# Kernel optimization log

Measured on AMD Instinct MI355X. Metric: run time of the kernel, lower is better.

The kernel has to match this reference:

```python
import jax, jax.numpy as jnp
import numpy as np

D_MODEL, D_K, D_V = 1024, 64, 64

def setup_inputs() -> dict:
    key = jax.random.key(0)
    ks = jax.random.split(key, 9)
    B, S = 8, 2048
    scale = 1.0 / np.sqrt(D_MODEL)
    return {
        "q_input": jax.random.normal(ks[0], (B, S, D_MODEL), jnp.float32),
        "k_input": jax.random.normal(ks[1], (B, S, D_MODEL), jnp.float32),
        "v_input": jax.random.normal(ks[2], (B, S, D_MODEL), jnp.float32),
        "Wq": jax.random.normal(ks[3], (D_K, D_MODEL), jnp.float32) * scale,
        "bq": jnp.zeros((D_K,), jnp.float32),
        "Wk": jax.random.normal(ks[4], (D_K, D_MODEL), jnp.float32) * scale,
        "bk": jnp.zeros((D_K,), jnp.float32),
        "Wv": jax.random.normal(ks[5], (D_V, D_MODEL), jnp.float32) * scale,
        "bv": jnp.zeros((D_V,), jnp.float32),
    }

def reference(q_input, k_input, v_input, Wq, bq, Wk, bk, Wv, bv):
    # Linear projections (torch Linear: x @ W^T + b)
    q = jnp.einsum('bsm,km->bsk', q_input, Wq) + bq  # [B,S,d_k]
    k = jnp.einsum('bsm,km->bsk', k_input, Wk) + bk  # [B,S,d_k]
    v = jnp.einsum('bsm,vm->bsv', v_input, Wv) + bv  # [B,S,d_v]
    scores = jnp.einsum('bqk,bsk->bqs', q, k) / jnp.sqrt(jnp.float32(D_K))
    # source applies causal mask unconditionally (is_mask is never None)
    S = q_input.shape[1]
    causal = jnp.tril(jnp.ones((S, S), bool))
    scores = jnp.where(causal[None], scores, jnp.float32(-1e9))
    attn = jax.nn.softmax(scores, axis=2)
    return jnp.einsum('bqs,bsv->bqv', attn, v)
```

## Files before the change

### kernel.cpp

```cpp
#include <hip/hip_runtime.h>
#include <hip/hip_bf16.h>

#define B_ 8
#define S_ 2048
#define DM 1024
#define DK 64

typedef __attribute__((ext_vector_type(8))) short bf16x8;
typedef __attribute__((ext_vector_type(4))) float f32x4;
typedef __attribute__((ext_vector_type(4))) short short4_t;
typedef unsigned int u32;

__device__ __forceinline__ short bf16s(float f) {
    union { float f; unsigned u; } v; v.f = f;
    unsigned r = v.u + 0x7fffu + ((v.u >> 16) & 1u);
    return (short)(r >> 16);
}

__global__ __launch_bounds__(256) void convw_kernel(
    const float* __restrict__ Wq, const float* __restrict__ Wk,
    const float* __restrict__ Wv, short* __restrict__ wbf)
{
    const int i = (blockIdx.x * 256 + threadIdx.x) * 8;
    const float* src = (i < 65536) ? Wq : (i < 131072) ? Wk : Wv;
    const int off = i & 65535;
    float4 f0 = *(const float4*)(src + off);
    float4 f1 = *(const float4*)(src + off + 4);
    bf16x8 o;
    o[0]=bf16s(f0.x); o[1]=bf16s(f0.y); o[2]=bf16s(f0.z); o[3]=bf16s(f0.w);
    o[4]=bf16s(f1.x); o[5]=bf16s(f1.y); o[6]=bf16s(f1.z); o[7]=bf16s(f1.w);
    *(bf16x8*)(wbf + i) = o;
}

__global__ __launch_bounds__(256) void proj_kernel(
    const float* __restrict__ xq, const float* __restrict__ xk, const float* __restrict__ xv,
    const short* __restrict__ wbf,
    const float* __restrict__ bq, const float* __restrict__ bk, const float* __restrict__ bv,
    short* __restrict__ q_ws, short* __restrict__ k_ws, short* __restrict__ vt_ws)
{
    __shared__ __align__(16) char smem[49152];

    const int which = blockIdx.y;
    const float* x    = (which == 0) ? xq : (which == 1) ? xk : xv;
    const float* bias = (which == 0) ? bq : (which == 1) ? bk : bv;
    const short* wsrc = wbf + which * (DK * DM);

    const int tid = threadIdx.x;
    const int w   = tid >> 6;
    const int i   = tid & 63;
    const int lr  = i & 15;
    const int g   = i >> 4;
    const int row0 = blockIdx.x * 64;

    const int rot = (blockIdx.x * 5 + which * 7) & 15;

    f32x4 acc[4];
    #pragma unroll
    for (int f = 0; f < 4; ++f) acc[f] = f32x4{0.f, 0.f, 0.f, 0.f};

    auto fetch = [&](f32x4 (&xb)[4], f32x4 (&wb)[2], int kc) {
        const float* xrow = x + (long)(row0 + w * 16) * DM + kc;
        #pragma unroll
        for (int j = 0; j < 4; ++j) {
            const int rl = j * 4 + g;
            xb[j] = __builtin_nontemporal_load(
                (const f32x4*)((const char*)(xrow + (long)rl * DM) + (i & 15) * 16));
        }
        const short* wrow = wsrc + (long)(w * 16) * DM + kc;
        #pragma unroll
        for (int j = 0; j < 2; ++j) {
            const int nl = j * 8 + (i >> 3);
            wb[j] = *(const f32x4*)((const char*)(wrow + (long)nl * DM) + (i & 7) * 16);
        }
    };
    auto writeLDS = [&](const f32x4 (&xb)[4], const f32x4 (&wb)[2], int buf) {
        char* xd = smem + buf * 16384 + (w * 16) * 256;
        #pragma unroll
        for (int j = 0; j < 4; ++j) {
            const int rl = j * 4 + g;
            *(f32x4*)(xd + rl * 256 + (((i & 15) * 16) ^ ((rl & 7) << 5))) = xb[j];
        }
        char* wd = smem + 32768 + buf * 8192 + (w * 16) * 128;
        #pragma unroll
        for (int j = 0; j < 2; ++j) {
            const int nl = j * 8 + (i >> 3);
            *(f32x4*)(wd + nl * 128 + (((i & 7) * 16) ^ ((nl & 7) << 4))) = wb[j];
        }
    };

    auto compute = [&](int buf) {
        const char* xr = smem + buf * 16384 + (w * 16 + lr) * 256;
        const char* wr = smem + 32768 + buf * 8192;
        const int sx = (lr & 7) << 5;
        const int sw = (lr & 7) << 4;
        #pragma unroll
        for (int ks = 0; ks < 2; ++ks) {
            const int bA = (ks * 128 + g * 32) ^ sx;
            f32x4 x0 = *(const f32x4*)(xr + bA);
            f32x4 x1 = *(const f32x4*)(xr + bA + 16);
            bf16x8 af;
            af[0]=bf16s(x0[0]); af[1]=bf16s(x0[1]); af[2]=bf16s(x0[2]); af[3]=bf16s(x0[3]);
            af[4]=bf16s(x1[0]); af[5]=bf16s(x1[1]); af[6]=bf16s(x1[2]); af[7]=bf16s(x1[3]);
            const int bB = (ks * 64 + g * 16) ^ sw;
            #pragma unroll
            for (int f = 0; f < 4; ++f) {
                bf16x8 wf = *(const bf16x8*)(wr + (f * 16 + lr) * 128 + bB);
                acc[f] = __builtin_amdgcn_mfma_f32_16x16x32_bf16(af, wf, acc[f], 0, 0, 0);
            }
        }
    };

    f32x4 xA[4], wA[2], xB[4], wB[2];
    fetch(xA, wA, rot * 64);
    writeLDS(xA, wA, 0);
    fetch(xB, wB, ((1 + rot) & 15) * 64);
    asm volatile("s_waitcnt lgkmcnt(0)" ::: "memory");
    asm volatile("s_barrier" ::: "memory");

    for (int t = 0; t < 16; t += 2) {
        compute(0);
        if (t + 2 < 16) fetch(xA, wA, ((t + 2 + rot) & 15) * 64);
        writeLDS(xB, wB, 1);
        asm volatile("s_waitcnt lgkmcnt(0)" ::: "memory");
        asm volatile("s_barrier" ::: "memory");
        compute(1);
        if (t + 3 < 16) fetch(xB, wB, ((t + 3 + rot) & 15) * 64);
        if (t + 2 < 16) {
            writeLDS(xA, wA, 0);
            asm volatile("s_waitcnt lgkmcnt(0)" ::: "memory");
        }
        asm volatile("s_barrier" ::: "memory");
    }

    if (which < 2) {
        short* stile = (short*)smem + w * 1024;
        #pragma unroll
        for (int f = 0; f < 4; ++f) {
            float bb = bias[f * 16 + lr];
            #pragma unroll
            for (int r = 0; r < 4; ++r)
                stile[(g * 4 + r) * 64 + f * 16 + lr] = bf16s(acc[f][r] + bb);
        }
        asm volatile("s_waitcnt lgkmcnt(0)" ::: "memory");
        __builtin_amdgcn_sched_barrier(0);
        short* outp = (which == 0) ? q_ws : k_ws;
        const long gbase = (long)(row0 + w * 16) * 64;
        *(bf16x8*)(outp + gbase +       i * 8) = *(const bf16x8*)(&stile[i * 8]);
        *(bf16x8*)(outp + gbase + 512 + i * 8) = *(const bf16x8*)(&stile[512 + i * 8]);
    } else {
        const int rw = row0 + w * 16;
        const int b = rw >> 11;
        const int s = (rw & 2047) + g * 4;
        #pragma unroll
        for (int f = 0; f < 4; ++f) {
            float bb = bias[f * 16 + lr];
            short4_t st;
            st[0]=bf16s(acc[f][0]+bb); st[1]=bf16s(acc[f][1]+bb);
            st[2]=bf16s(acc[f][2]+bb); st[3]=bf16s(acc[f][3]+bb);
            *(short4_t*)(vt_ws + (long)(b * 64 + f * 16 + lr) * S_ + s) = st;
        }
    }
}

__global__ __launch_bounds__(256) void attn_kernel(
    const short* __restrict__ q_ws, const short* __restrict__ k_ws,
    const short* __restrict__ vt_ws, float* __restrict__ out)
{
    __shared__ __align__(16) short plds[4][16 * 40];
    __shared__ __align__(16) float accds[4][64][16];
    __shared__ __align__(16) float2 mlds[4][16];

    const int n = blockIdx.x;
    const int c = n & 255, s = n >> 8;
    const int u = c & 127, v = c >> 7;
    const int b  = v * 4 + s;
    const int qt = (s & 1) ? (127 - u) : u;
    const int qbase = qt * 16;
    const int kend  = qbase + 16;
    const int niter = (kend + 31) >> 5;

    const int tid  = threadIdx.x;
    const int wv   = tid >> 6;
    const int lane = tid & 63;
    const int lr = lane & 15, g = lane >> 4, lk = g * 8;
    const int q_glob = qbase + lr;

    const short* qp = q_ws + ((long)b * S_ + qbase + lr) * DK;
    const bf16x8 qb0 = *(const bf16x8*)(qp + lk);
    const bf16x8 qb1 = *(const bf16x8*)(qp + 32 + lk);
    const short* kb = k_ws  + (long)b * S_ * DK;
    const short* vb = vt_ws + (long)b * DK * S_;

    float m = -INFINITY, l = 0.f;
    f32x4 acc[4];
    #pragma unroll
    for (int f = 0; f < 4; ++f) acc[f] = f32x4{0.f, 0.f, 0.f, 0.f};
    const float sc = 0.125f * 1.44269504088896340736f;

    short* pw = plds[wv];
    for (int t = wv; t < niter; t += 4) {
        const int kv = t * 32;
        const bool sub1 = (kv + 16) < kend;
        bf16x8 vf0 = *(const bf16x8*)(vb + (long)(lr)      * S_ + kv + lk);
        bf16x8 vf1 = *(const bf16x8*)(vb + (long)(16 + lr) * S_ + kv + lk);
        bf16x8 vf2 = *(const bf16x8*)(vb + (long)(32 + lr) * S_ + kv + lk);
        bf16x8 vf3 = *(const bf16x8*)(vb + (long)(48 + lr) * S_ + kv + lk);

        const short* kp0 = kb + (long)(kv + lr) * DK;
        bf16x8 k00 = *(const bf16x8*)(kp0 + lk);
        bf16x8 k01 = *(const bf16x8*)(kp0 + 32 + lk);
        f32x4 s0 = f32x4{0.f,0.f,0.f,0.f};
        s0 = __builtin_amdgcn_mfma_f32_16x16x32_bf16(k00, qb0, s0, 0, 0, 0);
        s0 = __builtin_amdgcn_mfma_f32_16x16x32_bf16(k01, qb1, s0, 0, 0, 0);
        f32x4 s1 = f32x4{0.f,0.f,0.f,0.f};
        if (sub1) {
            const short* kp1 = kp0 + 16 * DK;
            bf16x8 k10 = *(const bf16x8*)(kp1 + lk);
            bf16x8 k11 = *(const bf16x8*)(kp1 + 32 + lk);
            s1 = __builtin_amdgcn_mfma_f32_16x16x32_bf16(k10, qb0, s1, 0, 0, 0);
            s1 = __builtin_amdgcn_mfma_f32_16x16x32_bf16(k11, qb1, s1, 0, 0, 0);
        }

        float pv[8];
        #pragma unroll
        for (int r = 0; r < 4; ++r) {
            const int key0 = kv + g*4 + r;
            pv[r]     = (key0 <= q_glob) ? s0[r] * sc : -INFINITY;
            const int key1 = kv + 16 + g*4 + r;
            pv[4 + r] = (sub1 && key1 <= q_glob) ? s1[r] * sc : -INFINITY;
        }
        float tm = fmaxf(fmaxf(fmaxf(pv[0],pv[1]), fmaxf(pv[2],pv[3])),
                         fmaxf(fmaxf(pv[4],pv[5]), fmaxf(pv[6],pv[7])));
        tm = fmaxf(tm, __shfl_xor(tm, 16));
        tm = fmaxf(tm, __shfl_xor(tm, 32));
        const float mn  = fmaxf(m, tm);
        const float fac = exp2f(m - mn);
        float ps = 0.f;
        #pragma unroll
        for (int q = 0; q < 8; ++q) { pv[q] = exp2f(pv[q] - mn); ps += pv[q]; }
        ps += __shfl_xor(ps, 16);
        ps += __shfl_xor(ps, 32);
        l = l * fac + ps;
        m = mn;
        #pragma unroll
        for (int f = 0; f < 4; ++f)
            #pragma unroll
            for (int r = 0; r < 4; ++r) acc[f][r] *= fac;

        short4_t pw0, pw1;
        pw0[0]=bf16s(pv[0]); pw0[1]=bf16s(pv[1]); pw0[2]=bf16s(pv[2]); pw0[3]=bf16s(pv[3]);
        pw1[0]=bf16s(pv[4]); pw1[1]=bf16s(pv[5]); pw1[2]=bf16s(pv[6]); pw1[3]=bf16s(pv[7]);
        *(short4_t*)(pw + lr*40 + g*4)      = pw0;
        *(short4_t*)(pw + lr*40 + 16 + g*4) = pw1;
        asm volatile("s_waitcnt lgkmcnt(0)" ::: "memory");
        __builtin_amdgcn_sched_barrier(0);
        const bf16x8 pf = *(const bf16x8*)(pw + lr*40 + lk);

        acc[0] = __builtin_amdgcn_mfma_f32_16x16x32_bf16(vf0, pf, acc[0], 0, 0, 0);
        acc[1] = __builtin_amdgcn_mfma_f32_16x16x32_bf16(vf1, pf, acc[1], 0, 0, 0);
        acc[2] = __builtin_amdgcn_mfma_f32_16x16x32_bf16(vf2, pf, acc[2], 0, 0, 0);
        acc[3] = __builtin_amdgcn_mfma_f32_16x16x32_bf16(vf3, pf, acc[3], 0, 0, 0);
    }

    #pragma unroll
    for (int f = 0; f < 4; ++f)
        *(f32x4*)(&accds[wv][lane][f * 4]) = acc[f];
    if (g == 0) mlds[wv][lr] = float2{m, l};
    __syncthreads();

    const float2 ml0 = mlds[0][lr], ml1 = mlds[1][lr],
                 ml2 = mlds[2][lr], ml3 = mlds[3][lr];
    const float M = fmaxf(fmaxf(ml0.x, ml1.x), fmaxf(ml2.x, ml3.x));
    const float w0 = exp2f(ml0.x - M), w1 = exp2f(ml1.x - M),
                w2 = exp2f(ml2.x - M), w3 = exp2f(ml3.x - M);
    const float L = w0*ml0.y + w1*ml1.y + w2*ml2.y + w3*ml3.y;
    f32x4 o = w0 * (*(const f32x4*)(&accds[0][lane][wv * 4]))
            + w1 * (*(const f32x4*)(&accds[1][lane][wv * 4]))
            + w2 * (*(const f32x4*)(&accds[2][lane][wv * 4]))
            + w3 * (*(const f32x4*)(&accds[3][lane][wv * 4]));
    const float inv = 1.0f / L;
    o[0]*=inv; o[1]*=inv; o[2]*=inv; o[3]*=inv;
    *(f32x4*)(out + ((long)b * S_ + qbase + lr) * DK + wv * 16 + g * 4) = o;
}

extern "C" void kernel_launch(void* const* d_in, const int* in_sizes, int n_in,
                              void* d_out, int out_size, void* d_ws, size_t ws_size,
                              hipStream_t stream) {
    const float* q_in = (const float*)d_in[0];
    const float* k_in = (const float*)d_in[1];
    const float* v_in = (const float*)d_in[2];
    const float* Wq   = (const float*)d_in[3];
    const float* bq   = (const float*)d_in[4];
    const float* Wk   = (const float*)d_in[5];
    const float* bk   = (const float*)d_in[6];
    const float* Wv   = (const float*)d_in[7];
    const float* bv   = (const float*)d_in[8];

    short* q_ws  = (short*)d_ws;
    short* k_ws  = q_ws + (size_t)B_ * S_ * DK;
    short* vt_ws = k_ws + (size_t)B_ * S_ * DK;
    short* wbf   = vt_ws + (size_t)B_ * S_ * DK;
    float* out   = (float*)d_out;

    convw_kernel<<<dim3(96), 256, 0, stream>>>(Wq, Wk, Wv, wbf);
    proj_kernel<<<dim3((B_ * S_) / 64, 3), 256, 0, stream>>>(
        q_in, k_in, v_in, wbf, bq, bk, bv, q_ws, k_ws, vt_ws);
    attn_kernel<<<dim3(B_ * 128), 256, 0, stream>>>(q_ws, k_ws, vt_ws, out);
}
```

Measured before the change: 78.93 us.

## Split projection K-dimension across two wave halves with LDS reduction

```diff
diff --git a/kernel.cpp b/kernel.cpp
--- a/kernel.cpp
+++ b/kernel.cpp
@@ -32,7 +32,7 @@
     *(bf16x8*)(wbf + i) = o;
 }
 
-__global__ __launch_bounds__(256) void proj_kernel(
+__global__ __launch_bounds__(512) void proj_kernel(
     const float* __restrict__ xq, const float* __restrict__ xk, const float* __restrict__ xv,
     const short* __restrict__ wbf,
     const float* __restrict__ bq, const float* __restrict__ bk, const float* __restrict__ bv,
@@ -45,11 +45,13 @@
     const float* bias = (which == 0) ? bq : (which == 1) ? bk : bv;
     const short* wsrc = wbf + which * (DK * DM);
 
-    const int tid = threadIdx.x;
-    const int w   = tid >> 6;
-    const int i   = tid & 63;
-    const int lr  = i & 15;
-    const int g   = i >> 4;
+    const int tid  = threadIdx.x;
+    const int w8   = tid >> 6;
+    const int rowg = w8 >> 1;
+    const int kh   = w8 & 1;
+    const int i    = tid & 63;
+    const int lr   = i & 15;
+    const int g    = i >> 4;
     const int row0 = blockIdx.x * 64;
 
     const int rot = (blockIdx.x * 5 + which * 7) & 15;
@@ -58,73 +60,63 @@
     #pragma unroll
     for (int f = 0; f < 4; ++f) acc[f] = f32x4{0.f, 0.f, 0.f, 0.f};
 
-    auto fetch = [&](f32x4 (&xb)[4], f32x4 (&wb)[2], int kc) {
-        const float* xrow = x + (long)(row0 + w * 16) * DM + kc;
-        #pragma unroll
-        for (int j = 0; j < 4; ++j) {
-            const int rl = j * 4 + g;
+    auto fetch = [&](f32x4 (&xb)[2], f32x4 &wbv, int kc) {
+        const float* xrow = x + (long)(row0 + rowg * 16) * DM + kc;
+        #pragma unroll
+        for (int j = 0; j < 2; ++j) {
+            const int rl = j * 8 + (i >> 3);
             xb[j] = __builtin_nontemporal_load(
-                (const f32x4*)((const char*)(xrow + (long)rl * DM) + (i & 15) * 16));
-        }
-        const short* wrow = wsrc + (long)(w * 16) * DM + kc;
+                (const f32x4*)((const char*)(xrow + (long)rl * DM) + (i & 7) * 16));
+        }
+        const int n = rowg * 16 + (i >> 2);
+        wbv = *(const f32x4*)((const char*)(wsrc + (long)n * DM + kc) + (i & 3) * 16);
+    };
+    auto writeLDS = [&](const f32x4 (&xb)[2], const f32x4 &wbv, int buf) {
+        char* xd = smem + buf * 16384 + kh * 8192 + rowg * 2048;
         #pragma unroll
         for (int j = 0; j < 2; ++j) {
-            const int nl = j * 8 + (i >> 3);
-            wb[j] = *(const f32x4*)((const char*)(wrow + (long)nl * DM) + (i & 7) * 16);
-        }
+            const int rl = j * 8 + (i >> 3);
+            *(f32x4*)(xd + rl * 128 + (((i & 7) * 16) ^ ((rl & 7) << 4))) = xb[j];
+        }
+        char* wd = smem + 32768 + buf * 8192 + kh * 4096;
+        const int n = rowg * 16 + (i >> 2);
+        *(f32x4*)(wd + n * 64 + (((i & 3) * 16) ^ (((n >> 1) & 3) << 4))) = wbv;
     };
-    auto writeLDS = [&](const f32x4 (&xb)[4], const f32x4 (&wb)[2], int buf) {
-        char* xd = smem + buf * 16384 + (w * 16) * 256;
-        #pragma unroll
-        for (int j = 0; j < 4; ++j) {
-            const int rl = j * 4 + g;
-            *(f32x4*)(xd + rl * 256 + (((i & 15) * 16) ^ ((rl & 7) << 5))) = xb[j];
-        }
-        char* wd = smem + 32768 + buf * 8192 + (w * 16) * 128;
-        #pragma unroll
-        for (int j = 0; j < 2; ++j) {
-            const int nl = j * 8 + (i >> 3);
-            *(f32x4*)(wd + nl * 128 + (((i & 7) * 16) ^ ((nl & 7) << 4))) = wb[j];
+
+    auto compute = [&](int buf) {
+        const char* xr = smem + buf * 16384 + kh * 8192 + rowg * 2048 + lr * 128;
+        const char* wr = smem + 32768 + buf * 8192 + kh * 4096;
+        const int sx = (lr & 7) << 4;
+        f32x4 x0 = *(const f32x4*)(xr + ((g * 32) ^ sx));
+        f32x4 x1 = *(const f32x4*)(xr + ((g * 32 + 16) ^ sx));
+        bf16x8 af;
+        af[0]=bf16s(x0[0]); af[1]=bf16s(x0[1]); af[2]=bf16s(x0[2]); af[3]=bf16s(x0[3]);
+        af[4]=bf16s(x1[0]); af[5]=bf16s(x1[1]); af[6]=bf16s(x1[2]); af[7]=bf16s(x1[3]);
+        const int sw = ((lr >> 1) & 3) << 4;
+        #pragma unroll
+        for (int f = 0; f < 4; ++f) {
+            bf16x8 wf = *(const bf16x8*)(wr + (f * 16 + lr) * 64 + ((g * 16) ^ sw));
+            acc[f] = __builtin_amdgcn_mfma_f32_16x16x32_bf16(af, wf, acc[f], 0, 0, 0);
         }
     };
 
-    auto compute = [&](int buf) {
-        const char* xr = smem + buf * 16384 + (w * 16 + lr) * 256;
-        const char* wr = smem + 32768 + buf * 8192;
-        const int sx = (lr & 7) << 5;
-        const int sw = (lr & 7) << 4;
-        #pragma unroll
-        for (int ks = 0; ks < 2; ++ks) {
-            const int bA = (ks * 128 + g * 32) ^ sx;
-            f32x4 x0 = *(const f32x4*)(xr + bA);
-            f32x4 x1 = *(const f32x4*)(xr + bA + 16);
-            bf16x8 af;
-            af[0]=bf16s(x0[0]); af[1]=bf16s(x0[1]); af[2]=bf16s(x0[2]); af[3]=bf16s(x0[3]);
-            af[4]=bf16s(x1[0]); af[5]=bf16s(x1[1]); af[6]=bf16s(x1[2]); af[7]=bf16s(x1[3]);
-            const int bB = (ks * 64 + g * 16) ^ sw;
-            #pragma unroll
-            for (int f = 0; f < 4; ++f) {
-                bf16x8 wf = *(const bf16x8*)(wr + (f * 16 + lr) * 128 + bB);
-                acc[f] = __builtin_amdgcn_mfma_f32_16x16x32_bf16(af, wf, acc[f], 0, 0, 0);
-            }
-        }
-    };
-
-    f32x4 xA[4], wA[2], xB[4], wB[2];
-    fetch(xA, wA, rot * 64);
+    auto kcof = [&](int t) { return kh * 512 + ((t + rot) & 15) * 32; };
+
+    f32x4 xA[2], xB[2], wA, wB;
+    fetch(xA, wA, kcof(0));
     writeLDS(xA, wA, 0);
-    fetch(xB, wB, ((1 + rot) & 15) * 64);
+    fetch(xB, wB, kcof(1));
     asm volatile("s_waitcnt lgkmcnt(0)" ::: "memory");
     asm volatile("s_barrier" ::: "memory");
 
     for (int t = 0; t < 16; t += 2) {
         compute(0);
-        if (t + 2 < 16) fetch(xA, wA, ((t + 2 + rot) & 15) * 64);
+        if (t + 2 < 16) fetch(xA, wA, kcof(t + 2));
         writeLDS(xB, wB, 1);
         asm volatile("s_waitcnt lgkmcnt(0)" ::: "memory");
         asm volatile("s_barrier" ::: "memory");
         compute(1);
-        if (t + 3 < 16) fetch(xB, wB, ((t + 3 + rot) & 15) * 64);
+        if (t + 3 < 16) fetch(xB, wB, kcof(t + 3));
         if (t + 2 < 16) {
             writeLDS(xA, wA, 0);
             asm volatile("s_waitcnt lgkmcnt(0)" ::: "memory");
@@ -132,32 +124,50 @@
         asm volatile("s_barrier" ::: "memory");
     }
 
-    if (which < 2) {
-        short* stile = (short*)smem + w * 1024;
-        #pragma unroll
-        for (int f = 0; f < 4; ++f) {
-            float bb = bias[f * 16 + lr];
+    float* pacc = (float*)(smem + 16384);
+    if (kh == 1) {
+        #pragma unroll
+        for (int f = 0; f < 4; ++f)
             #pragma unroll
             for (int r = 0; r < 4; ++r)
-                stile[(g * 4 + r) * 64 + f * 16 + lr] = bf16s(acc[f][r] + bb);
-        }
-        asm volatile("s_waitcnt lgkmcnt(0)" ::: "memory");
-        __builtin_amdgcn_sched_barrier(0);
-        short* outp = (which == 0) ? q_ws : k_ws;
-        const long gbase = (long)(row0 + w * 16) * 64;
-        *(bf16x8*)(outp + gbase +       i * 8) = *(const bf16x8*)(&stile[i * 8]);
-        *(bf16x8*)(outp + gbase + 512 + i * 8) = *(const bf16x8*)(&stile[512 + i * 8]);
-    } else {
-        const int rw = row0 + w * 16;
-        const int b = rw >> 11;
-        const int s = (rw & 2047) + g * 4;
-        #pragma unroll
-        for (int f = 0; f < 4; ++f) {
-            float bb = bias[f * 16 + lr];
-            short4_t st;
-            st[0]=bf16s(acc[f][0]+bb); st[1]=bf16s(acc[f][1]+bb);
-            st[2]=bf16s(acc[f][2]+bb); st[3]=bf16s(acc[f][3]+bb);
-            *(short4_t*)(vt_ws + (long)(b * 64 + f * 16 + lr) * S_ + s) = st;
+                pacc[rowg * 1024 + (g * 4 + r) * 64 + f * 16 + lr] = acc[f][r];
+    }
+    asm volatile("s_waitcnt lgkmcnt(0)" ::: "memory");
+    asm volatile("s_barrier" ::: "memory");
+    if (kh == 0) {
+        #pragma unroll
+        for (int f = 0; f < 4; ++f)
+            #pragma unroll
+            for (int r = 0; r < 4; ++r)
+                acc[f][r] += pacc[rowg * 1024 + (g * 4 + r) * 64 + f * 16 + lr];
+
+        if (which < 2) {
+            short* stile = (short*)smem + rowg * 1024;
+            #pragma unroll
+            for (int f = 0; f < 4; ++f) {
+                float bb = bias[f * 16 + lr];
+                #pragma unroll
+                for (int r = 0; r < 4; ++r)
+                    stile[(g * 4 + r) * 64 + f * 16 + lr] = bf16s(acc[f][r] + bb);
+            }
+            asm volatile("s_waitcnt lgkmcnt(0)" ::: "memory");
+            __builtin_amdgcn_sched_barrier(0);
+            short* outp = (which == 0) ? q_ws : k_ws;
+            const long gbase = (long)(row0 + rowg * 16) * 64;
+            *(bf16x8*)(outp + gbase +       i * 8) = *(const bf16x8*)(&stile[i * 8]);
+            *(bf16x8*)(outp + gbase + 512 + i * 8) = *(const bf16x8*)(&stile[512 + i * 8]);
+        } else {
+            const int rw = row0 + rowg * 16;
+            const int b = rw >> 11;
+            const int s = (rw & 2047) + g * 4;
+            #pragma unroll
+            for (int f = 0; f < 4; ++f) {
+                float bb = bias[f * 16 + lr];
+                short4_t st;
+                st[0]=bf16s(acc[f][0]+bb); st[1]=bf16s(acc[f][1]+bb);
+                st[2]=bf16s(acc[f][2]+bb); st[3]=bf16s(acc[f][3]+bb);
+                *(short4_t*)(vt_ws + (long)(b * 64 + f * 16 + lr) * S_ + s) = st;
+            }
         }
     }
 }
@@ -303,7 +313,7 @@
     float* out   = (float*)d_out;
 
     convw_kernel<<<dim3(96), 256, 0, stream>>>(Wq, Wk, Wv, wbf);
-    proj_kernel<<<dim3((B_ * S_) / 64, 3), 256, 0, stream>>>(
+    proj_kernel<<<dim3((B_ * S_) / 64, 3), 512, 0, stream>>>(
         q_in, k_in, v_in, wbf, bq, bk, bv, q_ws, k_ws, vt_ws);
     attn_kernel<<<dim3(B_ * 128), 256, 0, stream>>>(q_ws, k_ws, vt_ws, out);
 }
```

New measurement: 83.46 us. +5.7%, slower.
